# Kernel optimization log

Measured on AMD Instinct MI355X. Metric: run time of the kernel, lower is better.

Reference implementation:

```python
import jax, jax.numpy as jnp
import numpy as np
import math

H, W = 1024, 1024

def setup_inputs() -> dict:
    key = jax.random.key(0)
    img = jax.random.uniform(key, (H, W), dtype=jnp.float32) * 255.0
    return {"InputImage": img}

def _phase_congruency(img):
    nrows, ncols = img.shape
    minWaveLength, mult = 3.0, 2.1
    nscale, norient = 5, 6
    sigmaOnf, k, cutOff, g = 0.55, 2.0, 0.5, 10.0
    eps = 1e-4

    cy, cx = nrows // 2, ncols // 2
    yy, xx = jnp.mgrid[0:nrows, 0:ncols]
    yy = (yy - cy) / nrows
    xx = (xx - cx) / ncols
    radius = jnp.sqrt(xx ** 2 + yy ** 2)
    radius = radius.at[cy, cx].set(1.0)
    theta = jnp.arctan2(-yy, xx)
    sintheta, costheta = jnp.sin(theta), jnp.cos(theta)

    # low-pass Butterworth (order 15, cutoff 0.45)
    normradius = radius / (jnp.abs(xx).max() * 2)
    lowpass = 1.0 / (1.0 + (normradius / 0.45) ** 30)

    # log-Gabor radial filters, [nscale, H, W]
    s = jnp.arange(nscale, dtype=jnp.float32)
    fo = 1.0 / (minWaveLength * mult ** s)            # [S]
    logGabor = jnp.exp(-jnp.log(radius[None] * (1.0 / fo)[:, None, None]) ** 2
                       / (2 * math.log(sigmaOnf) ** 2))
    annular = logGabor * lowpass[None]
    annular = annular.at[:, cy, cx].set(0.0)

    # angular spread, [norient, H, W]
    angl = jnp.arange(norient, dtype=jnp.float32) * (math.pi / norient)
    cosA, sinA = jnp.cos(angl), jnp.sin(angl)
    ds = sintheta[None] * cosA[:, None, None] - costheta[None] * sinA[:, None, None]
    dc = costheta[None] * cosA[:, None, None] + sintheta[None] * sinA[:, None, None]
    dtheta = jnp.minimum(jnp.abs(jnp.arctan2(ds, dc)) * (norient / 2), math.pi)
    spread = (jnp.cos(dtheta) + 1.0) / 2.0

    # full filter bank [O, S, H, W], shifted to DFT layout
    filt = jnp.fft.ifftshift(spread[:, None] * annular[None], axes=(-2, -1))

    F = jnp.fft.fft2(img)                              # complex64
    # cv2.idft is unscaled -> multiply numpy-style ifft by N
    z = jnp.fft.ifft2(filt * F[None, None]) * (nrows * ncols)   # [O,S,H,W]
    # original code: E (even) = channel 1 = Im(z), O (odd) = channel 0 = Re(z)
    E, O = z.imag, z.real
    An = jnp.abs(z)

    sumE = E.sum(axis=1)        # [O,H,W]
    sumO = O.sum(axis=1)
    sumAn = An.sum(axis=1)
    maxAn = An.max(axis=1)
    tau = jnp.median(An[:, 0].reshape(norient, -1), axis=1) / math.sqrt(math.log(4.0))

    XEnergy = jnp.sqrt(sumE ** 2 + sumO ** 2) + eps
    MeanE = sumE / XEnergy
    MeanO = sumO / XEnergy
    Energy = (E * MeanE[:, None] + O * MeanO[:, None]
              - jnp.abs(E * MeanO[:, None] - O * MeanE[:, None])).sum(axis=1)

    totalTau = tau * (1 - (1 / mult) ** nscale) / (1 - 1 / mult)   # [O]
    T = totalTau * math.sqrt(math.pi / 2) + k * totalTau * math.sqrt((4 - math.pi) / 2)
    Energy = jnp.maximum(Energy - T[:, None, None], 0.0)

    width = (sumAn / (maxAn + eps) - 1.0) / (nscale - 1)
    weight = 1.0 / (1.0 + jnp.exp((cutOff - width) * g))
    PC = weight * Energy / sumAn                       # [O,H,W]

    covx = PC * cosA[:, None, None]
    covy = PC * sinA[:, None, None]
    covx2 = (covx ** 2).sum(axis=0) / (norient / 2)
    covy2 = (covy ** 2).sum(axis=0) / (norient / 2)
    covxy = 4.0 * (covx * covy).sum(axis=0) / norient
    denom = jnp.sqrt(covxy ** 2 + (covx2 - covy2) ** 2) + eps
    M = (covy2 + covx2 + denom) / 2.0
    m = (covy2 + covx2 - denom) / 2.0
    return M, m

def reference(InputImage):
    M, m = _phase_congruency(InputImage)
    return (M, m)
```

## Files before the change

### kernel.cpp

```cpp
#include <hip/hip_runtime.h>
#include <math.h>

typedef float2 c2;

#define CSTR 1058

__device__ __forceinline__ c2 cmul(c2 a, c2 b){
  return make_float2(a.x*b.x - a.y*b.y, a.x*b.y + a.y*b.x);
}

__constant__ float2 c_tw32[16] = {
  {1.0f, 0.0f},
  {0.980785280f, 0.195090322f},
  {0.923879533f, 0.382683432f},
  {0.831469612f, 0.555570233f},
  {0.707106781f, 0.707106781f},
  {0.555570233f, 0.831469612f},
  {0.382683432f, 0.923879533f},
  {0.195090322f, 0.980785280f},
  {0.0f, 1.0f},
  {-0.195090322f, 0.980785280f},
  {-0.382683432f, 0.923879533f},
  {-0.555570233f, 0.831469612f},
  {-0.707106781f, 0.707106781f},
  {-0.831469612f, 0.555570233f},
  {-0.923879533f, 0.382683432f},
  {-0.980785280f, 0.195090322f}
};

__constant__ float c_lnfo[5]  = {1.0986123f, 1.8405496f, 2.5824700f, 3.3244106f, 4.0663219f};
__constant__ float c_angl[6]  = {0.0f, 0.5235988f, 1.0471976f, 1.5707963f, 2.0943951f, 2.6179939f};
__constant__ float c_cosA[6] = {1.0f, 0.8660254038f, 0.5f, 6.123233996e-17f, -0.5f, -0.8660254038f};
__constant__ float c_sinA[6] = {0.0f, 0.5f, 0.8660254038f, 1.0f, 0.8660254038f, 0.5f};

__device__ __forceinline__ constexpr int rev5(int k){
  return ((k&1)<<4) | ((k&2)<<2) | (k&4) | ((k&8)>>2) | ((k>>4)&1);
}

template<int SIGN, int M>
__device__ __forceinline__ void stage32(c2* r){
#pragma unroll
  for (int g = 0; g < 32; g += 2*M){
#pragma unroll
    for (int i = 0; i < M; ++i){
      const c2 a = r[g+i], b = r[g+i+M];
      r[g+i] = make_float2(a.x+b.x, a.y+b.y);
      c2 d = make_float2(a.x-b.x, a.y-b.y);
      if (i != 0){
        const float2 tt = c_tw32[i*(16/M)];
        d = cmul(d, make_float2(tt.x, (float)SIGN*tt.y));
      }
      r[g+i+M] = d;
    }
  }
}

template<int SIGN>
__device__ __forceinline__ void fft32(c2* r){
  stage32<SIGN,16>(r);
  stage32<SIGN,8>(r);
  stage32<SIGN,4>(r);
  stage32<SIGN,2>(r);
  stage32<SIGN,1>(r);
}

template<int SIGN>
__device__ __forceinline__ void fourstep_mid(c2* r, c2* line, int idx){
  const float ang = (float)SIGN * 0.006135923151542565f * (float)idx;
  c2 wst; sincosf(ang, &wst.y, &wst.x);
  c2 wc = make_float2(1.f, 0.f);
#pragma unroll
  for (int d = 0; d < 32; ++d){
    if ((d & 7) == 0 && d != 0){ float s, c; sincosf(ang*(float)d, &s, &c); wc = make_float2(c, s); }
    c2 v = r[rev5(d)];
    if (d != 0) v = cmul(v, wc);
    line[33*d + idx] = v;
    wc = cmul(wc, wst);
  }
  __syncthreads();
#pragma unroll
  for (int b = 0; b < 32; ++b) r[b] = line[33*idx + b];
  fft32<SIGN>(r);
}


template<int SIGN>
__global__ __launch_bounds__(256, 2) void k_col_fft(c2* __restrict__ Z){
  __shared__ c2 slab[8*CSTR];
  const int t = threadIdx.x;
  c2* base = Z + (size_t)blockIdx.y * 1048576;
  const int sub = t & 7, idx = t >> 3;
  const int col = blockIdx.x*8 + sub;
  c2 r[32];
#pragma unroll
  for (int a = 0; a < 32; ++a)
    r[a] = base[(size_t)(32*a + idx)*1024 + col];
  fft32<SIGN>(r);
  fourstep_mid<SIGN>(r, slab + sub*CSTR, idx);
#pragma unroll
  for (int c = 0; c < 32; ++c)
    base[(size_t)(32*c + idx)*1024 + col] = r[rev5(c)];
}

__global__ __launch_bounds__(256, 2) void k_row_fft_real(const float* __restrict__ in, c2* __restrict__ out){
  __shared__ c2 slab[8*CSTR];
  const int t = threadIdx.x;
  const int sub = t & 7, idx = t >> 3;
  const int row = blockIdx.x*8 + sub;
  const float* src = in + (size_t)row * 1024;
  c2* dst = out + (size_t)row * 1024;
  c2 r[32];
#pragma unroll
  for (int a = 0; a < 32; ++a)
    r[a] = make_float2(src[32*a + idx], 0.f);
  fft32<-1>(r);
  fourstep_mid<-1>(r, slab + sub*CSTR, idx);
#pragma unroll
  for (int c = 0; c < 32; ++c)
    dst[32*c + idx] = r[rev5(c)];
}

__global__ __launch_bounds__(256, 2) void k_row_ifft_filter(const c2* __restrict__ F, c2* __restrict__ Z,
                                                            const float* __restrict__ lnrT,
                                                            const float* __restrict__ thetaT, int slot0){
  __shared__ c2 slab[8*CSTR];
  const int t = threadIdx.x;
  const int sub = t & 7, idx = t >> 3;
  const int gslot = slot0 + blockIdx.y;
  const int orient = gslot / 5, scale = gslot - orient*5;
  const float lnfo = c_lnfo[scale], angl = c_angl[orient];
  const int row = blockIdx.x*8 + sub;
  const c2* src = F + (size_t)row * 1024;
  const float* lnrR = lnrT + (size_t)row * 1024;
  const float* thR  = thetaT + (size_t)row * 1024;
  c2* dst = Z + (size_t)blockIdx.y * 1048576 + (size_t)row * 1024;
  c2 r[32];
#pragma unroll
  for (int a = 0; a < 32; ++a){
    const int n = 32*a + idx;
    const c2 v = src[n];
    const float lnr = lnrR[n], th = thR[n];
    const float u = lnr + lnfo;
    const float lg = __expf(-u*u*1.3989572f);
    const float lp = 1.0f/(1.0f + __expf(fmaf(30.f, lnr, 23.955231f)));
    float d = th - angl;
    if (d <= -3.14159274f) d += 6.28318548f;
    const float dth = fminf(fabsf(d)*3.0f, 3.14159274f);
    const float f = lg*lp*0.5f*(__cosf(dth)+1.0f);
    r[a] = make_float2(v.x*f, v.y*f);
  }
  fft32<1>(r);
  fourstep_mid<1>(r, slab + sub*CSTR, idx);
#pragma unroll
  for (int c = 0; c < 32; ++c)
    dst[32*c + idx] = r[rev5(c)];
}

__global__ __launch_bounds__(256) void k_filt_tab(float* __restrict__ lnrT, float* __restrict__ thetaT){
  const int r = blockIdx.x;
  const int t = threadIdx.x;
  const float yy = (float)(r < 512 ? r : r - 1024) * (1.0f/1024.0f);
#pragma unroll
  for (int j = 0; j < 4; ++j){
    const int c = t + 256*j;
    const float xx = (float)(c < 512 ? c : c - 1024) * (1.0f/1024.0f);
    const float radius = sqrtf(xx*xx + yy*yy);
    float lnr = logf(radius);
    if (r == 0 && c == 0) lnr = __int_as_float(0x7F800000);
    lnrT[r*1024 + c] = lnr;
    thetaT[r*1024 + c] = atan2f(-yy, xx);
  }
}


__device__ __forceinline__ unsigned amp_bits(const c2 v){
  return __float_as_uint(sqrtf(v.x*v.x + v.y*v.y));
}

__global__ __launch_bounds__(256) void k_med_p1b(const c2* __restrict__ Zb, size_t oStride,
                                                 unsigned* __restrict__ g1, int oBase){
  __shared__ unsigned h[4][4096];
  const int t = threadIdx.x;
  const int wv = t >> 6;
  const c2* z0 = Zb + (size_t)blockIdx.y * oStride;
  unsigned* gg = g1 + (size_t)(oBase + blockIdx.y) * 4096;
  for (int j = t; j < 4*4096; j += 256) ((unsigned*)h)[j] = 0;
  __syncthreads();
  const int base = blockIdx.x * 16384;
  for (int it = 0; it < 64; ++it){
    const unsigned bits = amp_bits(z0[base + it*256 + t]);
    atomicAdd(&h[wv][bits >> 20], 1u);
  }
  __syncthreads();
  for (int j = t; j < 4096; j += 256){
    const unsigned s = h[0][j] + h[1][j] + h[2][j] + h[3][j];
    if (s) atomicAdd(&gg[j], s);
  }
}

__global__ __launch_bounds__(256) void k_sel1b(const unsigned* __restrict__ g1,
                                               unsigned* __restrict__ sc1,
                                               unsigned* __restrict__ g2, int oBase){
  __shared__ unsigned partial[256];
  const int t = threadIdx.x;
  const int oo = oBase + blockIdx.x;
  const unsigned* gg = g1 + (size_t)oo * 4096;
  unsigned loc[16]; unsigned s = 0;
#pragma unroll
  for (int j = 0; j < 16; ++j){ loc[j] = gg[t*16 + j]; s += loc[j]; }
  partial[t] = s;
  __syncthreads();
  unsigned p = 0;
  for (int u = 0; u < t; ++u) p += partial[u];
  for (int which = 0; which < 2; ++which){
    const unsigned R = 524287u + (unsigned)which;
    if (R >= p && R - p < s){
      unsigned cum = p;
      for (int j = 0; j < 16; ++j){
        if (R - cum < loc[j]){ sc1[oo*4 + which*2] = (unsigned)(t*16 + j); sc1[oo*4 + which*2+1] = R - cum; break; }
        cum += loc[j];
      }
    }
  }
  for (int j = t; j < 8192; j += 256) g2[(size_t)oo*8192 + j] = 0;
}

__global__ __launch_bounds__(256) void k_med_p2b(const c2* __restrict__ Zb, size_t oStride,
                                                 const unsigned* __restrict__ sc1,
                                                 unsigned* __restrict__ g2, int oBase){
  __shared__ unsigned h[2][4096];
  const int t = threadIdx.x;
  const int oo = oBase + blockIdx.y;
  const c2* z0 = Zb + (size_t)blockIdx.y * oStride;
  unsigned* gg = g2 + (size_t)oo * 8192;
  for (int j = t; j < 8192; j += 256) ((unsigned*)h)[j] = 0;
  __syncthreads();
  const unsigned b0 = sc1[oo*4 + 0], b1 = sc1[oo*4 + 2];
  const int base = blockIdx.x * 16384;
  for (int it = 0; it < 64; ++it){
    const unsigned bits = amp_bits(z0[base + it*256 + t]);
    const unsigned top = bits >> 20;
    const unsigned mid = (bits >> 8) & 4095u;
    if (top == b0)      atomicAdd(&h[0][mid], 1u);
    else if (top == b1) atomicAdd(&h[1][mid], 1u);
  }
  __syncthreads();
  for (int j = t; j < 4096; j += 256){
    if (h[0][j]) atomicAdd(&gg[j], h[0][j]);
    if (h[1][j]) atomicAdd(&gg[4096 + j], h[1][j]);
  }
}

__global__ __launch_bounds__(256) void k_sel2b(const unsigned* __restrict__ g2,
                                               const unsigned* __restrict__ sc1,
                                               unsigned* __restrict__ sc2,
                                               unsigned* __restrict__ g3, int oBase){
  __shared__ unsigned partial[256];
  const int t = threadIdx.x;
  const int oo = oBase + blockIdx.x;
  const unsigned b0 = sc1[oo*4+0], lr0 = sc1[oo*4+1], b1 = sc1[oo*4+2], lr1 = sc1[oo*4+3];
  for (int which = 0; which < 2; ++which){
    const unsigned* hh = g2 + (size_t)oo*8192 + ((which == 1 && b1 != b0) ? 4096 : 0);
    const unsigned R = which ? lr1 : lr0;
    unsigned loc[16]; unsigned s = 0;
#pragma unroll
    for (int j = 0; j < 16; ++j){ loc[j] = hh[t*16 + j]; s += loc[j]; }
    partial[t] = s;
    __syncthreads();
    unsigned p = 0;
    for (int u = 0; u < t; ++u) p += partial[u];
    if (R >= p && R - p < s){
      unsigned cum = p;
      for (int j = 0; j < 16; ++j){
        if (R - cum < loc[j]){ sc2[oo*4 + which*2] = (unsigned)(t*16 + j); sc2[oo*4 + which*2+1] = R - cum; break; }
        cum += loc[j];
      }
    }
    __syncthreads();
  }
  for (int j = t; j < 512; j += 256) g3[(size_t)oo*512 + j] = 0;
}

__global__ __launch_bounds__(256) void k_med_p3b(const c2* __restrict__ Zb, size_t oStride,
                                                 const unsigned* __restrict__ sc1,
                                                 const unsigned* __restrict__ sc2,
                                                 unsigned* __restrict__ g3, int oBase){
  __shared__ unsigned h[2][256];
  const int t = threadIdx.x;
  const int oo = oBase + blockIdx.y;
  const c2* z0 = Zb + (size_t)blockIdx.y * oStride;
  unsigned* gg = g3 + (size_t)oo * 512;
  h[0][t] = 0; h[1][t] = 0;
  __syncthreads();
  const unsigned k0 = (sc1[oo*4+0] << 12) | sc2[oo*4+0];
  const unsigned k1 = (sc1[oo*4+2] << 12) | sc2[oo*4+2];
  const int base = blockIdx.x * 16384;
  for (int it = 0; it < 64; ++it){
    const unsigned bits = amp_bits(z0[base + it*256 + t]);
    const unsigned key = bits >> 8;
    if (key == k0)       atomicAdd(&h[0][bits & 255u], 1u);
    else if (key == k1)  atomicAdd(&h[1][bits & 255u], 1u);
  }
  __syncthreads();
  if (h[0][t]) atomicAdd(&gg[t], h[0][t]);
  if (h[1][t]) atomicAdd(&gg[256 + t], h[1][t]);
}

__global__ __launch_bounds__(256) void k_sel3b(const unsigned* __restrict__ g3,
                                               const unsigned* __restrict__ sc1,
                                               const unsigned* __restrict__ sc2,
                                               float* __restrict__ Tval, int oBase){
  __shared__ unsigned partial[256];
  __shared__ float vres[2];
  const int t = threadIdx.x;
  const int oo = oBase + blockIdx.x;
  const unsigned k0 = (sc1[oo*4+0] << 12) | sc2[oo*4+0];
  const unsigned k1 = (sc1[oo*4+2] << 12) | sc2[oo*4+2];
  for (int which = 0; which < 2; ++which){
    const unsigned* hh = g3 + (size_t)oo*512 + ((which == 1 && k1 != k0) ? 256 : 0);
    const unsigned R = which ? sc2[oo*4+3] : sc2[oo*4+1];
    partial[t] = hh[t];
    __syncthreads();
    unsigned p = 0;
    for (int u = 0; u < t; ++u) p += partial[u];
    if (R >= p && R - p < partial[t]){
      const unsigned key = which ? k1 : k0;
      vres[which] = __uint_as_float((key << 8) | (unsigned)t);
    }
    __syncthreads();
  }
  if (t == 0){
    const float med = 0.5f * (vres[0] + vres[1]);
    const float tau = med / 1.17741001f;
    const float totalTau = tau * 1.8623464f;
    const float T = totalTau * 1.25331414f + 2.0f * totalTau * 0.65513638f;
    Tval[oo] = T;
  }
}


__global__ __launch_bounds__(256) void k_pix_all(const c2* __restrict__ Z, const float* __restrict__ Tval,
                                                 float* __restrict__ out){
  const int i = blockIdx.x * 256 + threadIdx.x;
  float covx2 = 0.f, covy2 = 0.f, covxy = 0.f;
#pragma unroll
  for (int o = 0; o < 6; ++o){
    const float T = Tval[o];
    float E[5], O[5];
    float sumE = 0.f, sumO = 0.f, sumAn = 0.f, maxAn = 0.f;
#pragma unroll
    for (int s = 0; s < 5; ++s){
      const c2 z = Z[(size_t)(o*5 + s) * 1048576 + i];
      O[s] = z.x; E[s] = z.y;
      const float an = sqrtf(z.x*z.x + z.y*z.y);
      sumE += E[s]; sumO += O[s]; sumAn += an; maxAn = fmaxf(maxAn, an);
    }
    const float XE = sqrtf(sumE*sumE + sumO*sumO) + 1e-4f;
    const float ME = sumE / XE, MO = sumO / XE;
    float energy = 0.f;
#pragma unroll
    for (int s = 0; s < 5; ++s)
      energy += E[s]*ME + O[s]*MO - fabsf(E[s]*MO - O[s]*ME);
    energy = fmaxf(energy - T, 0.f);
    const float width = (sumAn / (maxAn + 1e-4f) - 1.0f) * 0.25f;
    const float weight = 1.0f / (1.0f + expf((0.5f - width) * 10.0f));
    const float PC = weight * energy / sumAn;
    const float cx = PC * c_cosA[o], cy = PC * c_sinA[o];
    covx2 += cx*cx; covy2 += cy*cy; covxy += cx*cy;
  }
  covx2 *= (1.0f/3.0f);
  covy2 *= (1.0f/3.0f);
  covxy *= (4.0f/6.0f);
  const float dnm = sqrtf(covxy*covxy + (covx2 - covy2)*(covx2 - covy2)) + 1e-4f;
  const float ss = covy2 + covx2;
  out[i] = (ss + dnm) / 2.0f;
  out[1048576 + i] = (ss - dnm) / 2.0f;
}


__global__ __launch_bounds__(256) void k_pix(const c2* __restrict__ Z, const float* __restrict__ Tp,
                                             float cA, float sA,
                                             float* __restrict__ ax2, float* __restrict__ ay2,
                                             float* __restrict__ axy, int first){
  const int i = blockIdx.x * 256 + threadIdx.x;
  const float T = *Tp;
  float E[5], O[5];
  float sumE = 0.f, sumO = 0.f, sumAn = 0.f, maxAn = 0.f;
#pragma unroll
  for (int s = 0; s < 5; ++s){
    const c2 z = Z[(size_t)s * 1048576 + i];
    O[s] = z.x; E[s] = z.y;
    const float an = sqrtf(z.x*z.x + z.y*z.y);
    sumE += E[s]; sumO += O[s]; sumAn += an; maxAn = fmaxf(maxAn, an);
  }
  const float XE = sqrtf(sumE*sumE + sumO*sumO) + 1e-4f;
  const float ME = sumE / XE, MO = sumO / XE;
  float energy = 0.f;
#pragma unroll
  for (int s = 0; s < 5; ++s)
    energy += E[s]*ME + O[s]*MO - fabsf(E[s]*MO - O[s]*ME);
  energy = fmaxf(energy - T, 0.f);
  const float width = (sumAn / (maxAn + 1e-4f) - 1.0f) * 0.25f;
  const float weight = 1.0f / (1.0f + expf((0.5f - width) * 10.0f));
  const float PC = weight * energy / sumAn;
  const float cx = PC * cA, cy = PC * sA;
  if (first){ ax2[i] = cx*cx; ay2[i] = cy*cy; axy[i] = cx*cy; }
  else      { ax2[i] += cx*cx; ay2[i] += cy*cy; axy[i] += cx*cy; }
}

__global__ __launch_bounds__(256) void k_final(const float* __restrict__ ax2, const float* __restrict__ ay2,
                                               const float* __restrict__ axy, float* __restrict__ out){
  const int i = blockIdx.x * 256 + threadIdx.x;
  const float cx2 = ax2[i] / 3.0f;
  const float cy2 = ay2[i] / 3.0f;
  const float cxy = 4.0f * axy[i] / 6.0f;
  const float dnm = sqrtf(cxy*cxy + (cx2 - cy2)*(cx2 - cy2)) + 1e-4f;
  const float ss = cy2 + cx2;
  out[i] = (ss + dnm) / 2.0f;
  out[1048576 + i] = (ss - dnm) / 2.0f;
}

extern "C" void kernel_launch(void* const* d_in, const int* in_sizes, int n_in,
                              void* d_out, int out_size, void* d_ws, size_t ws_size,
                              hipStream_t stream){
  (void)in_sizes; (void)n_in; (void)out_size;
  const float* img = (const float*)d_in[0];
  float* out = (float*)d_out;
  char* w = (char*)d_ws;

  const dim3 th(256);

  if (ws_size >= (size_t)268435456){
    c2* F  = (c2*)(w);
    c2* Z  = (c2*)(w + 8388608);
    float* lnrT   = (float*)(w + 260046848);
    float* thetaT = (float*)(w + 264241152);
    unsigned* g1  = (unsigned*)(w);
    unsigned* g2  = (unsigned*)(w + 98304);
    unsigned* g3  = (unsigned*)(w + 294912);
    unsigned* sc1 = (unsigned*)(w + 307200);
    unsigned* sc2 = (unsigned*)(w + 307328);
    float* Tval   = (float*)(w + 307456);

    k_filt_tab<<<dim3(1024), th, 0, stream>>>(lnrT, thetaT);

    k_row_fft_real<<<dim3(128), th, 0, stream>>>(img, F);
    k_col_fft<-1><<<dim3(128, 1), th, 0, stream>>>(F);

    k_row_ifft_filter<<<dim3(128, 30), th, 0, stream>>>(F, Z, lnrT, thetaT, 0);
    k_col_fft<1><<<dim3(128, 30), th, 0, stream>>>(Z);

    hipMemsetAsync(g1, 0, 6*16384, stream);
    const size_t oStride = (size_t)5 * 1048576;
    k_med_p1b<<<dim3(64, 6), th, 0, stream>>>(Z, oStride, g1, 0);
    k_sel1b<<<dim3(6), th, 0, stream>>>(g1, sc1, g2, 0);
    k_med_p2b<<<dim3(64, 6), th, 0, stream>>>(Z, oStride, sc1, g2, 0);
    k_sel2b<<<dim3(6), th, 0, stream>>>(g2, sc1, sc2, g3, 0);
    k_med_p3b<<<dim3(64, 6), th, 0, stream>>>(Z, oStride, sc1, sc2, g3, 0);
    k_sel3b<<<dim3(6), th, 0, stream>>>(g3, sc1, sc2, Tval, 0);

    k_pix_all<<<dim3(4096), th, 0, stream>>>(Z, Tval, out);
  } else {
    c2* F   = (c2*)(w);
    c2* C5  = (c2*)(w + 8388608);
    float* lnrT   = (float*)(w + 50331648);
    float* thetaT = (float*)(w + 54525952);
    float* ax2 = (float*)(w + 58720256);
    float* ay2 = ax2 + 1048576;
    float* axy = ay2 + 1048576;
    unsigned* g1  = (unsigned*)(w + 71303168);
    unsigned* g2  = (unsigned*)(w + 71319552);
    unsigned* g3  = (unsigned*)(w + 71352320);
    unsigned* sc1 = (unsigned*)(w + 71354368);
    unsigned* sc2 = (unsigned*)(w + 71354496);
    float* Tval   = (float*)(w + 71354624);

    k_filt_tab<<<dim3(1024), th, 0, stream>>>(lnrT, thetaT);
    k_row_fft_real<<<dim3(128), th, 0, stream>>>(img, F);
    k_col_fft<-1><<<dim3(128, 1), th, 0, stream>>>(F);

    for (int o = 0; o < 6; ++o){
      k_row_ifft_filter<<<dim3(128, 5), th, 0, stream>>>(F, C5, lnrT, thetaT, o*5);
      k_col_fft<1><<<dim3(128, 5), th, 0, stream>>>(C5);

      hipMemsetAsync(g1, 0, 16384, stream);
      k_med_p1b<<<dim3(64, 1), th, 0, stream>>>(C5, 0, g1, 0);
      k_sel1b<<<dim3(1), th, 0, stream>>>(g1, sc1, g2, 0);
      k_med_p2b<<<dim3(64, 1), th, 0, stream>>>(C5, 0, sc1, g2, 0);
      k_sel2b<<<dim3(1), th, 0, stream>>>(g2, sc1, sc2, g3, 0);
      k_med_p3b<<<dim3(64, 1), th, 0, stream>>>(C5, 0, sc1, sc2, g3, 0);
      k_sel3b<<<dim3(1), th, 0, stream>>>(g3, sc1, sc2, Tval, 0);

      const double a = (double)o * (M_PI/6.0);
      k_pix<<<dim3(4096), th, 0, stream>>>(C5, Tval, (float)cos(a), (float)sin(a),
                                           ax2, ay2, axy, (o == 0) ? 1 : 0);
    }
    k_final<<<dim3(4096), th, 0, stream>>>(ax2, ay2, axy, out);
  }
}
```

Measured before the change: 469.4 us.

## Replace row FFT kernels with shared-memory radix-4 1024-point FFT reusing filter terms across scales

The row FFT kernels move from a register four-step scheme (32x32 with a transpose slab) to a whole-row Stockham radix-4 FFT in shared memory, using XOR-swizzled indices to avoid bank conflicts and per-thread precomputed twiddles. The inverse filter kernel now processes one orientation per block and loops over the 5 scales. The F row, log-radius and the lowpass*spread product are loaded and computed once, then reused for every scale, which cuts repeated global loads and transcendental work. The cost is 5 barriers per FFT stage sequence and much more shared memory per block, which may lower occupancy. Each block also walks through 4 rows serially.

Measured after the change: 391.6 us, median of 2. 1.2x faster.

```diff
diff --git a/kernel.cpp b/kernel.cpp
--- a/kernel.cpp
+++ b/kernel.cpp
@@ -3,6 +3,7 @@
 
 typedef float2 c2;
 
+#define S_IDX(i) ((i) ^ (((i) >> 5) & 15))
 #define CSTR 1058
 
 __device__ __forceinline__ c2 cmul(c2 a, c2 b){
@@ -33,6 +34,54 @@
 __constant__ float c_cosA[6] = {1.0f, 0.8660254038f, 0.5f, 6.123233996e-17f, -0.5f, -0.8660254038f};
 __constant__ float c_sinA[6] = {0.0f, 0.5f, 0.8660254038f, 1.0f, 0.8660254038f, 0.5f};
 
+
+template<int SIGN>
+__device__ __forceinline__ void make_tw3(int t, c2* w1, c2* w2, c2* w3){
+#pragma unroll
+  for (int k = 0; k < 5; ++k){
+    const int s = 1 << (2*k);
+    const float ang = (float)SIGN * 0.00613592315154256f * (float)(t & ~(s-1));
+    sincosf(ang, &w1[k].y, &w1[k].x);
+    w2[k] = cmul(w1[k], w1[k]);
+    w3[k] = cmul(w2[k], w1[k]);
+  }
+}
+
+template<int SIGN>
+__device__ __forceinline__ void fft1024(c2* bufA, c2* bufB, int t,
+                                        const c2* w1a, const c2* w2a, const c2* w3a){
+  c2* cur = bufA; c2* oth = bufB;
+#pragma unroll
+  for (int k = 0; k < 5; ++k){
+    const int s = 1 << (2*k);
+    const int q = t & (s - 1);
+    c2 a = cur[S_IDX(t)];
+    c2 b = cur[S_IDX(t + 256)];
+    c2 c = cur[S_IDX(t + 512)];
+    c2 d = cur[S_IDX(t + 768)];
+    c2 apc = make_float2(a.x + c.x, a.y + c.y);
+    c2 amc = make_float2(a.x - c.x, a.y - c.y);
+    c2 bpd = make_float2(b.x + d.x, b.y + d.y);
+    c2 bmd = make_float2(b.x - d.x, b.y - d.y);
+    c2 y0 = make_float2(apc.x + bpd.x, apc.y + bpd.y);
+    c2 e2 = make_float2(apc.x - bpd.x, apc.y - bpd.y);
+    const float S4 = (float)SIGN;
+    c2 u1 = make_float2(amc.x - S4*bmd.y, amc.y + S4*bmd.x);
+    c2 u3 = make_float2(amc.x + S4*bmd.y, amc.y - S4*bmd.x);
+    c2 y1 = cmul(u1, w1a[k]);
+    c2 y2 = cmul(e2, w2a[k]);
+    c2 y3 = cmul(u3, w3a[k]);
+    const int bw = 4*t - 3*q;
+    oth[S_IDX(bw)]       = y0;
+    oth[S_IDX(bw + s)]   = y1;
+    oth[S_IDX(bw + 2*s)] = y2;
+    oth[S_IDX(bw + 3*s)] = y3;
+    c2* tmp = cur; cur = oth; oth = tmp;
+    __syncthreads();
+  }
+}
+
+
 __device__ __forceinline__ constexpr int rev5(int k){
   return ((k&1)<<4) | ((k&2)<<2) | (k&4) | ((k&8)>>2) | ((k>>4)&1);
 }
@@ -83,7 +132,6 @@
   fft32<SIGN>(r);
 }
 
-
 template<int SIGN>
 __global__ __launch_bounds__(256, 2) void k_col_fft(c2* __restrict__ Z){
   __shared__ c2 slab[8*CSTR];
@@ -102,59 +150,6 @@
     base[(size_t)(32*c + idx)*1024 + col] = r[rev5(c)];
 }
 
-__global__ __launch_bounds__(256, 2) void k_row_fft_real(const float* __restrict__ in, c2* __restrict__ out){
-  __shared__ c2 slab[8*CSTR];
-  const int t = threadIdx.x;
-  const int sub = t & 7, idx = t >> 3;
-  const int row = blockIdx.x*8 + sub;
-  const float* src = in + (size_t)row * 1024;
-  c2* dst = out + (size_t)row * 1024;
-  c2 r[32];
-#pragma unroll
-  for (int a = 0; a < 32; ++a)
-    r[a] = make_float2(src[32*a + idx], 0.f);
-  fft32<-1>(r);
-  fourstep_mid<-1>(r, slab + sub*CSTR, idx);
-#pragma unroll
-  for (int c = 0; c < 32; ++c)
-    dst[32*c + idx] = r[rev5(c)];
-}
-
-__global__ __launch_bounds__(256, 2) void k_row_ifft_filter(const c2* __restrict__ F, c2* __restrict__ Z,
-                                                            const float* __restrict__ lnrT,
-                                                            const float* __restrict__ thetaT, int slot0){
-  __shared__ c2 slab[8*CSTR];
-  const int t = threadIdx.x;
-  const int sub = t & 7, idx = t >> 3;
-  const int gslot = slot0 + blockIdx.y;
-  const int orient = gslot / 5, scale = gslot - orient*5;
-  const float lnfo = c_lnfo[scale], angl = c_angl[orient];
-  const int row = blockIdx.x*8 + sub;
-  const c2* src = F + (size_t)row * 1024;
-  const float* lnrR = lnrT + (size_t)row * 1024;
-  const float* thR  = thetaT + (size_t)row * 1024;
-  c2* dst = Z + (size_t)blockIdx.y * 1048576 + (size_t)row * 1024;
-  c2 r[32];
-#pragma unroll
-  for (int a = 0; a < 32; ++a){
-    const int n = 32*a + idx;
-    const c2 v = src[n];
-    const float lnr = lnrR[n], th = thR[n];
-    const float u = lnr + lnfo;
-    const float lg = __expf(-u*u*1.3989572f);
-    const float lp = 1.0f/(1.0f + __expf(fmaf(30.f, lnr, 23.955231f)));
-    float d = th - angl;
-    if (d <= -3.14159274f) d += 6.28318548f;
-    const float dth = fminf(fabsf(d)*3.0f, 3.14159274f);
-    const float f = lg*lp*0.5f*(__cosf(dth)+1.0f);
-    r[a] = make_float2(v.x*f, v.y*f);
-  }
-  fft32<1>(r);
-  fourstep_mid<1>(r, slab + sub*CSTR, idx);
-#pragma unroll
-  for (int c = 0; c < 32; ++c)
-    dst[32*c + idx] = r[rev5(c)];
-}
 
 __global__ __launch_bounds__(256) void k_filt_tab(float* __restrict__ lnrT, float* __restrict__ thetaT){
   const int r = blockIdx.x;
@@ -169,6 +164,80 @@
     if (r == 0 && c == 0) lnr = __int_as_float(0x7F800000);
     lnrT[r*1024 + c] = lnr;
     thetaT[r*1024 + c] = atan2f(-yy, xx);
+  }
+}
+
+__global__ __launch_bounds__(256) void k_fft_fwd_real(const float* __restrict__ in, c2* __restrict__ out){
+  const int t = threadIdx.x;
+  __shared__ c2 bufA[1024];
+  __shared__ c2 bufB[1024];
+  c2 w1[5], w2[5], w3[5]; make_tw3<-1>(t, w1, w2, w3);
+  for (int rr = 0; rr < 4; ++rr){
+    const int row = blockIdx.x * 4 + rr;
+    const float* src = in + (size_t)row * 1024;
+    c2* dst = out + (size_t)row * 1024;
+#pragma unroll
+    for (int j = 0; j < 4; ++j){
+      const int q = t + 256*j;
+      bufA[S_IDX(q)] = make_float2(src[q], 0.0f);
+    }
+    __syncthreads();
+    fft1024<-1>(bufA, bufB, t, w1, w2, w3);
+#pragma unroll
+    for (int j = 0; j < 4; ++j){ const int q = t + 256*j; dst[q] = bufB[S_IDX(q)]; }
+    __syncthreads();
+  }
+}
+
+__global__ __launch_bounds__(256) void k_fft_inv_filter_g(const c2* __restrict__ F, c2* __restrict__ Z,
+                                                          const float* __restrict__ lnrT,
+                                                          const float* __restrict__ thetaT, int orient0){
+  const int t = threadIdx.x;
+  const int orient = orient0 + blockIdx.y;
+  const float angl = c_angl[orient];
+  __shared__ c2 bufA[1024];
+  __shared__ c2 bufB[1024];
+  __shared__ c2 Frow[1024];
+  __shared__ float commSh[1024];
+  __shared__ float lnrSh[1024];
+  c2 w1[5], w2[5], w3[5]; make_tw3<1>(t, w1, w2, w3);
+  for (int rr = 0; rr < 4; ++rr){
+    const int row = blockIdx.x * 4 + rr;
+    const c2* src = F + (size_t)row * 1024;
+    const float* lnrR = lnrT + (size_t)row * 1024;
+    const float* thR  = thetaT + (size_t)row * 1024;
+#pragma unroll
+    for (int j = 0; j < 4; ++j){
+      const int q = t + 256*j;
+      Frow[q] = src[q];
+      const float lnr = lnrR[q];
+      const float th  = thR[q];
+      const float lp = 1.0f/(1.0f + __expf(fmaf(30.f, lnr, 23.955231f)));
+      float d = th - angl;
+      if (d <= -3.14159274f) d += 6.28318548f;
+      const float dth = fminf(fabsf(d)*3.0f, 3.14159274f);
+      const float spr = 0.5f*(__cosf(dth)+1.0f);
+      lnrSh[q] = lnr;
+      commSh[q] = lp*spr;
+    }
+    __syncthreads();
+    for (int s = 0; s < 5; ++s){
+      const float lnfo = c_lnfo[s];
+      c2* dst = Z + ((size_t)blockIdx.y*5 + s) * 1048576 + (size_t)row * 1024;
+#pragma unroll
+      for (int j = 0; j < 4; ++j){
+        const int q = t + 256*j;
+        const float u = lnrSh[q] + lnfo;
+        const float f = __expf(-u*u*1.3989572f) * commSh[q];
+        const c2 v = Frow[q];
+        bufA[S_IDX(q)] = make_float2(v.x*f, v.y*f);
+      }
+      __syncthreads();
+      fft1024<1>(bufA, bufB, t, w1, w2, w3);
+#pragma unroll
+      for (int j = 0; j < 4; ++j){ const int q = t + 256*j; dst[q] = bufB[S_IDX(q)]; }
+      __syncthreads();
+    }
   }
 }
 
@@ -444,13 +513,13 @@
 
     k_filt_tab<<<dim3(1024), th, 0, stream>>>(lnrT, thetaT);
 
-    k_row_fft_real<<<dim3(128), th, 0, stream>>>(img, F);
+    k_fft_fwd_real<<<dim3(256), th, 0, stream>>>(img, F);
     k_col_fft<-1><<<dim3(128, 1), th, 0, stream>>>(F);
 
-    k_row_ifft_filter<<<dim3(128, 30), th, 0, stream>>>(F, Z, lnrT, thetaT, 0);
+    k_fft_inv_filter_g<<<dim3(256, 6), th, 0, stream>>>(F, Z, lnrT, thetaT, 0);
+    hipMemsetAsync(g1, 0, 6*16384, stream);
     k_col_fft<1><<<dim3(128, 30), th, 0, stream>>>(Z);
 
-    hipMemsetAsync(g1, 0, 6*16384, stream);
     const size_t oStride = (size_t)5 * 1048576;
     k_med_p1b<<<dim3(64, 6), th, 0, stream>>>(Z, oStride, g1, 0);
     k_sel1b<<<dim3(6), th, 0, stream>>>(g1, sc1, g2, 0);
@@ -476,14 +545,14 @@
     float* Tval   = (float*)(w + 71354624);
 
     k_filt_tab<<<dim3(1024), th, 0, stream>>>(lnrT, thetaT);
-    k_row_fft_real<<<dim3(128), th, 0, stream>>>(img, F);
+    k_fft_fwd_real<<<dim3(256), th, 0, stream>>>(img, F);
     k_col_fft<-1><<<dim3(128, 1), th, 0, stream>>>(F);
 
     for (int o = 0; o < 6; ++o){
-      k_row_ifft_filter<<<dim3(128, 5), th, 0, stream>>>(F, C5, lnrT, thetaT, o*5);
+      k_fft_inv_filter_g<<<dim3(256, 1), th, 0, stream>>>(F, C5, lnrT, thetaT, o);
+      hipMemsetAsync(g1, 0, 16384, stream);
       k_col_fft<1><<<dim3(128, 5), th, 0, stream>>>(C5);
 
-      hipMemsetAsync(g1, 0, 16384, stream);
       k_med_p1b<<<dim3(64, 1), th, 0, stream>>>(C5, 0, g1, 0);
       k_sel1b<<<dim3(1), th, 0, stream>>>(g1, sc1, g2, 0);
       k_med_p2b<<<dim3(64, 1), th, 0, stream>>>(C5, 0, sc1, g2, 0);
```
